# Optimization experiments

Hardware: AMD Instinct MI355X
Metric: run time of the kernel (lower is better)

Reference implementation:

```python
import jax, jax.numpy as jnp
import numpy as np
from jax import lax

SUB_NO = 20
T_NO = 401       # odd, so padding=T_NO//2 preserves length
N_E = 2000
N_I = 200
T_DATA = 50000
EXP_NO = 81
HID_NO = 6


def _conv1d(x, kern, pad, groups=1):
    # x: [N, C, L], kern: [O, I, K]; torch-style cross-correlation
    return lax.conv_general_dilated(
        x, kern, window_strides=(1,), padding=[(pad, pad)],
        dimension_numbers=('NCH', 'OIH', 'NCH'), feature_group_count=groups)


def setup_inputs() -> dict:
    key = jax.random.key(0)
    ks = jax.random.split(key, 8)
    rng = np.random.default_rng(0)

    # binary-tree dendrite: parent(j) = (j-1)//2; C_den[parent, child] = 1
    C_den = np.zeros((SUB_NO, SUB_NO), np.float32)
    for j in range(1, SUB_NO):
        C_den[(j - 1) // 2, j] = 1.0

    # one-hot synapse -> subunit assignment matrices
    C_syn_e = np.zeros((SUB_NO, N_E), np.float32)
    C_syn_e[rng.integers(0, SUB_NO, N_E), np.arange(N_E)] = 1.0
    C_syn_i = np.zeros((SUB_NO, N_I), np.float32)
    C_syn_i[rng.integers(0, SUB_NO, N_I), np.arange(N_I)] = 1.0

    # Gaussian-bump temporal basis (fixed buffer)
    raw = np.arange(T_NO, dtype=np.float32)
    points = np.arange(0, 5 * EXP_NO, 5, dtype=np.float32)
    exp_basis = np.exp(-(raw[None, :] - points[:, None]) ** 2 / 30.0).astype(np.float32)

    f32 = jnp.float32
    return {
        'S_e': jax.random.uniform(ks[0], (T_DATA, N_E), dtype=f32),
        'S_i': jax.random.uniform(ks[1], (T_DATA, N_I), dtype=f32),
        'Z': jax.random.bernoulli(ks[2], 0.02, (T_DATA,)).astype(f32),
        'W_syn': jax.random.normal(ks[3], (SUB_NO, 2), dtype=f32) * 0.01,
        'Tau_syn': jnp.ones((SUB_NO, 2), f32) * 3.0,
        'Delta_syn': jnp.ones((SUB_NO, 2), f32),
        'W_sub': jnp.ones((SUB_NO,), f32) * 0.1,
        'W_spk': jnp.ones((1,), f32),
        'Tau_spk': jnp.ones((1,), f32) * 3.0,
        'Theta': jnp.zeros((SUB_NO,), f32),
        'W_root_1': jax.random.normal(ks[4], (HID_NO, 1, EXP_NO), dtype=f32) * 0.01,
        'W_root_2': jax.random.normal(ks[5], (1, HID_NO, EXP_NO), dtype=f32) * 0.01,
        'C_den': jnp.asarray(C_den),
        'C_syn_e': jnp.asarray(C_syn_e),
        'C_syn_i': jnp.asarray(C_syn_i),
        'exp_basis': jnp.asarray(exp_basis),
    }


def reference(S_e, S_i, Z, W_syn, Tau_syn, Delta_syn, W_sub, W_spk, Tau_spk,
              Theta, W_root_1, W_root_2, C_den, C_syn_e, C_syn_i, exp_basis):
    T = S_e.shape[0]
    sub_no = C_den.shape[0]
    T_no = exp_basis.shape[1]

    # ---- spike_convolve ----
    syn_e = S_e @ C_syn_e.T          # [T, sub]
    syn_i = S_i @ C_syn_i.T          # [T, sub]

    t = jnp.arange(T_no, dtype=S_e.dtype)[None, :]            # [1, T_no]
    t_e = jnp.maximum(t - Delta_syn[:, 0:1], 0.0)
    t_i = jnp.maximum(t - Delta_syn[:, 1:2], 0.0)
    t_tau_e = t_e / Tau_syn[:, 0:1] ** 2
    t_tau_i = t_i / Tau_syn[:, 1:2] ** 2
    full_e_kern = t_tau_e * jnp.exp(-t_tau_e) * W_syn[:, 0:1] ** 2     # [sub, T_no]
    full_i_kern = -(t_tau_i * jnp.exp(-t_tau_i) * W_syn[:, 1:2] ** 2)  # [sub, T_no]

    ke = jnp.flip(full_e_kern, 1)[:, None, :]   # [sub, 1, T_no]
    ki = jnp.flip(full_i_kern, 1)[:, None, :]

    pad_e = jnp.pad(syn_e, ((T_no - 1, 0), (0, 0))).T[None]  # [1, sub, T+T_no-1]
    pad_i = jnp.pad(syn_i, ((T_no - 1, 0), (0, 0))).T[None]
    filt_e = _conv1d(pad_e, ke, 0, groups=sub_no)[0].T        # [T, sub]
    filt_i = _conv1d(pad_i, ki, 0, groups=sub_no)[0].T
    syn = filt_e + filt_i
    out_filters = jnp.concatenate([full_e_kern, full_i_kern], axis=0)  # [2*sub, T_no]

    # ---- subunit tree recursion (children have larger indices than parents) ----
    root_kern_1 = jnp.flip(jnp.matmul(W_root_1, exp_basis), 2)  # [hid, 1, T_no]
    root_kern_2 = jnp.flip(jnp.matmul(W_root_2, exp_basis), 2)  # [1, hid, T_no]
    w2 = W_sub ** 2

    ns_out = jnp.zeros((T, sub_no), S_e.dtype)
    for i in range(sub_no - 1, 0, -1):
        child = ns_out @ (C_den[i] * w2)                 # [T]
        ns_out = ns_out.at[:, i].set(jnp.tanh(syn[:, i] + Theta[i] + child))

    # root subunit with 2-layer temporal conv head
    child = ns_out @ (C_den[0] * w2)
    ns_in = syn[:, 0] + Theta[0] + child
    h = jnp.tanh(ns_in)[None, None, :]                   # [1, 1, T]
    h = jnp.tanh(_conv1d(h, root_kern_1, T_no // 2))     # [1, hid, T]
    final_Z = jax.nn.sigmoid(_conv1d(h, root_kern_2, T_no // 2).reshape(-1))  # [T]

    # ---- spike-history filter on Z ----
    t1 = jnp.arange(T_no, dtype=S_e.dtype)
    t_tau = t1 / Tau_spk ** 2
    spk_kern = jnp.flip(t_tau * jnp.exp(-t_tau) * W_spk ** 2, 0)[None, None, :]
    pad_Z = jnp.pad(Z, (T_no, 0))[None, None, :]         # [1, 1, T+T_no]
    final_V = _conv1d(pad_Z, spk_kern, 0).reshape(-1)[:-1]   # [T]

    return (final_V, final_Z, out_filters)
```

## Files before the change

### kernel.cpp

```cpp
#include <hip/hip_runtime.h>
#include <math.h>

#define T_DATA 50000
#define N_E 2000
#define N_I 200
#define SUB_NO 20
#define T_NO 401
#define KP 404
#define EXP_NO 81
#define HID_NO 6
#define ROWS 16

#define WS_SYN_ET   0
#define WS_SYN_IT   1000000
#define WS_SYNT     2000000
#define WS_H0       3000000
#define WS_H        3050000
#define WS_PART     3350000
#define WS_KE       3650000
#define WS_KI       3658080
#define WS_K1       3666160
#define WS_K2       3668584
#define WS_SPK      3671008
#define WS_ASGE     3671412
#define WS_ASGI     3671924

__global__ __launch_bounds__(256) void k_prep(
    const float* __restrict__ W_syn, const float* __restrict__ Tau_syn,
    const float* __restrict__ Delta_syn, const float* __restrict__ W_spk,
    const float* __restrict__ Tau_spk, const float* __restrict__ W_root_1,
    const float* __restrict__ W_root_2, const float* __restrict__ C_syn_e,
    const float* __restrict__ C_syn_i, const float* __restrict__ exp_basis,
    float* __restrict__ ws, unsigned int* __restrict__ asg_e,
    unsigned int* __restrict__ asg_i, float* __restrict__ out_filters) {
  const int bid = blockIdx.x, tid = threadIdx.x;
  if (bid == 0) {
    for (int u = tid; u < 512; u += 256) {
      unsigned int p = 0;
      for (int jj = 0; jj < 4; ++jj) {
        const int e = u * 4 + jj;
        int a = 20;
        if (e < N_E) {
          a = 0;
          for (int s = 0; s < SUB_NO; ++s) if (C_syn_e[s * N_E + e] > 0.5f) a = s;
        }
        p |= (unsigned int)a << (8 * jj);
      }
      asg_e[u] = p;
    }
  } else if (bid == 1) {
    for (int u = tid; u < 64; u += 256) {
      unsigned int p = 0;
      for (int jj = 0; jj < 4; ++jj) {
        const int e = u * 4 + jj;
        int a = 20;
        if (e < N_I) {
          a = 0;
          for (int s = 0; s < SUB_NO; ++s) if (C_syn_i[s * N_I + e] > 0.5f) a = s;
        }
        p |= (unsigned int)a << (8 * jj);
      }
      asg_i[u] = p;
    }
  } else if (bid == 2) {
    const float tau = Tau_spk[0], w = W_spk[0];
    const float it2 = 1.f / (tau * tau);
    for (int t = tid; t < KP; t += 256) {
      float v = 0.f;
      if (t < T_NO) { float tt = (float)t * it2; v = tt * __expf(-tt) * w * w; }
      ws[WS_SPK + t] = v;
    }
  } else if (bid < 3 + SUB_NO) {
    const int s = bid - 3;
    const float we = W_syn[s * 2], wi = W_syn[s * 2 + 1];
    const float te = Tau_syn[s * 2], ti = Tau_syn[s * 2 + 1];
    const float de = Delta_syn[s * 2], di = Delta_syn[s * 2 + 1];
    const float ie2 = 1.f / (te * te), ii2 = 1.f / (ti * ti);
    for (int t = tid; t < KP; t += 256) {
      float ve = 0.f, vi = 0.f;
      if (t < T_NO) {
        float xe = fmaxf((float)t - de, 0.f) * ie2;
        float xi = fmaxf((float)t - di, 0.f) * ii2;
        ve = xe * __expf(-xe) * we * we;
        vi = -(xi * __expf(-xi) * wi * wi);
        out_filters[s * T_NO + t] = ve;
        out_filters[(SUB_NO + s) * T_NO + t] = vi;
      }
      ws[WS_KE + s * KP + t] = ve;
      ws[WS_KI + s * KP + t] = vi;
    }
  } else {
    const int h = bid - (3 + SUB_NO);
    for (int t = tid; t < KP; t += 256) {
      float v1 = 0.f, v2 = 0.f;
      if (t < T_NO) {
        for (int b = 0; b < EXP_NO; ++b) {
          float bb = exp_basis[b * T_NO + t];
          v1 = fmaf(W_root_1[h * EXP_NO + b], bb, v1);
          v2 = fmaf(W_root_2[h * EXP_NO + b], bb, v2);
        }
      }
      ws[WS_K1 + h * KP + t] = v1;
      ws[WS_K2 + h * KP + t] = v2;
    }
  }
}

#define TSTR 260
__global__ __launch_bounds__(256) void k_seg(
    const float* __restrict__ S_e, const float* __restrict__ S_i,
    const unsigned int* __restrict__ asg_e, const unsigned int* __restrict__ asg_i,
    float* __restrict__ syn_eT, float* __restrict__ syn_iT) {
  __shared__ __align__(16) float tile[ROWS * TSTR];
  __shared__ float acc[256 * 21];
  __shared__ unsigned int asgl[512 + 64];
  const int tid = threadIdx.x;
  const int t0 = blockIdx.x * ROWS;
  const int r = tid & 15;
  const int sub = tid >> 4;
  float* __restrict__ myacc = acc + tid * 21;

  for (int i = tid; i < 512; i += 256) asgl[i] = asg_e[i];
  if (tid < 64) asgl[512 + tid] = asg_i[tid];
  #pragma unroll
  for (int i = 0; i < 21; ++i) myacc[i] = 0.f;
  __syncthreads();

  for (int ch = 0; ch < 8; ++ch) {
    #pragma unroll
    for (int i = 0; i < 4; ++i) {
      const int g = tid + i * 256;
      const int row = g >> 6, c4 = g & 63;
      const int col = ch * 256 + c4 * 4;
      float4 v = make_float4(0.f, 0.f, 0.f, 0.f);
      if (col < N_E) v = *(const float4*)(S_e + (size_t)(t0 + row) * N_E + col);
      *(float4*)(tile + row * TSTR + c4 * 4) = v;
    }
    __syncthreads();
    #pragma unroll
    for (int j = 0; j < 4; ++j) {
      const float4 v = *(const float4*)(tile + r * TSTR + sub * 16 + j * 4);
      const unsigned int a = asgl[ch * 64 + sub * 4 + j];
      myacc[a & 255] += v.x;
      myacc[(a >> 8) & 255] += v.y;
      myacc[(a >> 16) & 255] += v.z;
      myacc[a >> 24] += v.w;
    }
    __syncthreads();
  }
  for (int o = tid; o < ROWS * SUB_NO; o += 256) {
    const int row = o & 15, s = o >> 4;
    float sum = 0.f;
    #pragma unroll
    for (int c = 0; c < 16; ++c) sum += acc[(c * 16 + row) * 21 + s];
    syn_eT[s * T_DATA + t0 + row] = sum;
  }
  __syncthreads();
  #pragma unroll
  for (int i = 0; i < 21; ++i) myacc[i] = 0.f;

  #pragma unroll
  for (int i = 0; i < 4; ++i) {
    const int g = tid + i * 256;
    const int row = g >> 6, c4 = g & 63;
    const int col = c4 * 4;
    float4 v = make_float4(0.f, 0.f, 0.f, 0.f);
    if (col < N_I) v = *(const float4*)(S_i + (size_t)(t0 + row) * N_I + col);
    *(float4*)(tile + row * TSTR + c4 * 4) = v;
  }
  __syncthreads();
  #pragma unroll
  for (int j = 0; j < 4; ++j) {
    const float4 v = *(const float4*)(tile + r * TSTR + sub * 16 + j * 4);
    const unsigned int a = asgl[512 + sub * 4 + j];
    myacc[a & 255] += v.x;
    myacc[(a >> 8) & 255] += v.y;
    myacc[(a >> 16) & 255] += v.z;
    myacc[a >> 24] += v.w;
  }
  __syncthreads();
  for (int o = tid; o < ROWS * SUB_NO; o += 256) {
    const int row = o & 15, s = o >> 4;
    float sum = 0.f;
    #pragma unroll
    for (int c = 0; c < 16; ++c) sum += acc[(c * 16 + row) * 21 + s];
    syn_iT[s * T_DATA + t0 + row] = sum;
  }
}

template <int NOUT>
__device__ __forceinline__ void conv_acc(const float* __restrict__ xl,
                                         const float* __restrict__ kg,
                                         int lt, float* __restrict__ acc) {
  constexpr int NW = NOUT + 4;
  float xw[NW];
  #pragma unroll
  for (int r = 0; r < NW / 4; ++r) {
    float4 v = *(const float4*)(xl + lt + 400 + 4 * r);
    xw[4 * r + 0] = v.x; xw[4 * r + 1] = v.y;
    xw[4 * r + 2] = v.z; xw[4 * r + 3] = v.w;
  }
  const float* kp = kg;
  for (int g = 0; g < 100; ++g) {
    float4 kv = *(const float4*)kp; kp += 4;
    float kw[4] = {kv.x, kv.y, kv.z, kv.w};
    #pragma unroll
    for (int m = 0; m < 4; ++m)
      #pragma unroll
      for (int j = 0; j < NOUT; ++j)
        acc[j] = fmaf(kw[m], xw[4 + j - m], acc[j]);
    #pragma unroll
    for (int i = NW - 1; i >= 4; --i) xw[i] = xw[i - 4];
    float4 nv = *(const float4*)(xl + lt + 396 - 4 * g);
    xw[0] = nv.x; xw[1] = nv.y; xw[2] = nv.z; xw[3] = nv.w;
  }
  {
    float4 kv = *(const float4*)kp;
    float kw[4] = {kv.x, kv.y, kv.z, kv.w};
    #pragma unroll
    for (int m = 0; m < 4; ++m)
      #pragma unroll
      for (int j = 0; j < NOUT; ++j)
        acc[j] = fmaf(kw[m], xw[4 + j - m], acc[j]);
  }
}

__device__ __forceinline__ void fill_tile(float* __restrict__ xl,
                                          const float* __restrict__ X,
                                          int o, int n) {
  for (int i = threadIdx.x; i < n; i += blockDim.x) {
    int g = o + i;
    xl[i] = (g >= 0 && g < T_DATA) ? X[g] : 0.f;
  }
}

__global__ __launch_bounds__(256) void k_syn_conv(
    const float* __restrict__ syn_eT, const float* __restrict__ syn_iT,
    const float* __restrict__ ws, float* __restrict__ synT) {
  const int s = blockIdx.y;
  const int t0 = blockIdx.x * 2048;
  __shared__ __align__(16) float xe[2456];
  __shared__ __align__(16) float xi[2456];
  fill_tile(xe, syn_eT + s * T_DATA, t0 - 404, 2452);
  fill_tile(xi, syn_iT + s * T_DATA, t0 - 404, 2452);
  __syncthreads();
  const int lt = threadIdx.x * 8;
  float acc[8] = {0, 0, 0, 0, 0, 0, 0, 0};
  conv_acc<8>(xe, ws + WS_KE + s * KP, lt, acc);
  conv_acc<8>(xi, ws + WS_KI + s * KP, lt, acc);
  const int t = t0 + lt;
  #pragma unroll
  for (int j = 0; j < 8; ++j)
    if (t + j < T_DATA) synT[s * T_DATA + t + j] = acc[j];
}

__global__ __launch_bounds__(256) void k_tree(
    const float* __restrict__ synT, const float* __restrict__ Theta,
    const float* __restrict__ W_sub, float* __restrict__ h0) {
  const int t = blockIdx.x * 256 + threadIdx.x;
  if (t >= T_DATA) return;
  float ns[SUB_NO];
  #pragma unroll
  for (int i = SUB_NO - 1; i >= 1; --i) {
    float x = synT[i * T_DATA + t] + Theta[i];
    const int c1 = 2 * i + 1, c2 = 2 * i + 2;
    if (c1 < SUB_NO) { float w = W_sub[c1]; x = fmaf(w * w, ns[c1], x); }
    if (c2 < SUB_NO) { float w = W_sub[c2]; x = fmaf(w * w, ns[c2], x); }
    ns[i] = tanhf(x);
  }
  const float w1 = W_sub[1], w2 = W_sub[2];
  const float x0 = synT[t] + Theta[0] + w1 * w1 * ns[1] + w2 * w2 * ns[2];
  h0[t] = tanhf(x0);
}

__global__ __launch_bounds__(256) void k_root1(
    const float* __restrict__ h0, const float* __restrict__ ws,
    float* __restrict__ h_ws) {
  const int c = blockIdx.y;
  const int t0 = blockIdx.x * 1024;
  __shared__ __align__(16) float xt[1432];
  fill_tile(xt, h0, t0 + 200 - 404, 1428);
  __syncthreads();
  const int lt = threadIdx.x * 4;
  float acc[4] = {0, 0, 0, 0};
  conv_acc<4>(xt, ws + WS_K1 + c * KP, lt, acc);
  const int t = t0 + lt;
  #pragma unroll
  for (int j = 0; j < 4; ++j)
    if (t + j < T_DATA) h_ws[c * T_DATA + t + j] = tanhf(acc[j]);
}

__global__ __launch_bounds__(256) void k_root2(
    const float* __restrict__ h_ws, const float* __restrict__ ws,
    float* __restrict__ part) {
  const int c = blockIdx.y;
  const int t0 = blockIdx.x * 1024;
  __shared__ __align__(16) float xt[1432];
  fill_tile(xt, h_ws + c * T_DATA, t0 + 200 - 404, 1428);
  __syncthreads();
  const int lt = threadIdx.x * 4;
  float acc[4] = {0, 0, 0, 0};
  conv_acc<4>(xt, ws + WS_K2 + c * KP, lt, acc);
  const int t = t0 + lt;
  #pragma unroll
  for (int j = 0; j < 4; ++j)
    if (t + j < T_DATA) part[c * T_DATA + t + j] = acc[j];
}

__global__ __launch_bounds__(256) void k_comb(
    const float* __restrict__ part, float* __restrict__ outZ) {
  const int t = blockIdx.x * 256 + threadIdx.x;
  if (t >= T_DATA) return;
  float v = 0.f;
  #pragma unroll
  for (int c = 0; c < HID_NO; ++c) v += part[c * T_DATA + t];
  outZ[t] = 1.f / (1.f + __expf(-v));
}

__global__ __launch_bounds__(256) void k_spk(
    const float* __restrict__ Z, const float* __restrict__ ws,
    float* __restrict__ outV) {
  const int t0 = blockIdx.x * 1024;
  __shared__ __align__(16) float xt[1432];
  fill_tile(xt, Z, t0 - 1 - 404, 1428);
  __syncthreads();
  const int lt = threadIdx.x * 4;
  float acc[4] = {0, 0, 0, 0};
  conv_acc<4>(xt, ws + WS_SPK, lt, acc);
  const int t = t0 + lt;
  #pragma unroll
  for (int j = 0; j < 4; ++j)
    if (t + j < T_DATA) outV[t + j] = acc[j];
}

extern "C" void kernel_launch(void* const* d_in, const int* in_sizes, int n_in,
                              void* d_out, int out_size, void* d_ws, size_t ws_size,
                              hipStream_t stream) {
  const float* S_e      = (const float*)d_in[0];
  const float* S_i      = (const float*)d_in[1];
  const float* Z        = (const float*)d_in[2];
  const float* W_syn    = (const float*)d_in[3];
  const float* Tau_syn  = (const float*)d_in[4];
  const float* Delta_syn= (const float*)d_in[5];
  const float* W_sub    = (const float*)d_in[6];
  const float* W_spk    = (const float*)d_in[7];
  const float* Tau_spk  = (const float*)d_in[8];
  const float* Theta    = (const float*)d_in[9];
  const float* W_root_1 = (const float*)d_in[10];
  const float* W_root_2 = (const float*)d_in[11];
  const float* C_syn_e  = (const float*)d_in[13];
  const float* C_syn_i  = (const float*)d_in[14];
  const float* exp_basis= (const float*)d_in[15];

  float* ws = (float*)d_ws;
  unsigned int* asg_e = (unsigned int*)(ws + WS_ASGE);
  unsigned int* asg_i = (unsigned int*)(ws + WS_ASGI);
  float* out = (float*)d_out;

  k_prep<<<3 + SUB_NO + HID_NO, 256, 0, stream>>>(
      W_syn, Tau_syn, Delta_syn, W_spk, Tau_spk, W_root_1, W_root_2,
      C_syn_e, C_syn_i, exp_basis, ws, asg_e, asg_i, out + 2 * T_DATA);

  k_seg<<<T_DATA / ROWS, 256, 0, stream>>>(
      S_e, S_i, asg_e, asg_i, ws + WS_SYN_ET, ws + WS_SYN_IT);

  k_syn_conv<<<dim3(25, SUB_NO), 256, 0, stream>>>(
      ws + WS_SYN_ET, ws + WS_SYN_IT, ws, ws + WS_SYNT);

  k_tree<<<(T_DATA + 255) / 256, 256, 0, stream>>>(
      ws + WS_SYNT, Theta, W_sub, ws + WS_H0);

  k_root1<<<dim3(49, HID_NO), 256, 0, stream>>>(ws + WS_H0, ws, ws + WS_H);

  k_root2<<<dim3(49, HID_NO), 256, 0, stream>>>(ws + WS_H, ws, ws + WS_PART);

  k_comb<<<(T_DATA + 255) / 256, 256, 0, stream>>>(ws + WS_PART, out + T_DATA);

  k_spk<<<49, 256, 0, stream>>>(Z, ws, out);
}
```

Baseline: 191.5 us.

## Load S_e directly to registers, split syn conv by e/i, merge spike conv, fast tanh

The segment-sum kernel now reads S_e/S_i rows straight from global memory into registers instead of staging through a shared tile, which removes two barriers per chunk. The synaptic conv is split into separate excitatory and inhibitory blocks to double parallelism, and the tree kernel sums the two results. The spike-history conv is folded into the root2 launch as an extra grid row, and tanh and sigmoid use fast exp/rcp intrinsics. Trade-offs: the direct global loads are less coalesced across threads, the split conv needs an extra intermediate buffer, and the fast math lowers accuracy.

```diff
diff --git a/kernel.cpp b/kernel.cpp
--- a/kernel.cpp
+++ b/kernel.cpp
@@ -13,17 +13,23 @@
 
 #define WS_SYN_ET   0
 #define WS_SYN_IT   1000000
-#define WS_SYNT     2000000
-#define WS_H0       3000000
-#define WS_H        3050000
-#define WS_PART     3350000
-#define WS_KE       3650000
-#define WS_KI       3658080
-#define WS_K1       3666160
-#define WS_K2       3668584
-#define WS_SPK      3671008
-#define WS_ASGE     3671412
-#define WS_ASGI     3671924
+#define WS_SYNTE    2000000
+#define WS_SYNTI    3000000
+#define WS_H0       4000000
+#define WS_H        4050000
+#define WS_PART     4350000
+#define WS_KE       4650000
+#define WS_KI       4658080
+#define WS_K1       4666160
+#define WS_K2       4668584
+#define WS_SPK      4671008
+#define WS_ASGE     4671412
+#define WS_ASGI     4671924
+
+__device__ __forceinline__ float ftanh(float x) {
+  float e = __expf(2.f * x);
+  return 1.f - 2.f * __builtin_amdgcn_rcpf(e + 1.f);
+}
 
 __global__ __launch_bounds__(256) void k_prep(
     const float* __restrict__ W_syn, const float* __restrict__ Tau_syn,
@@ -106,18 +112,16 @@
   }
 }
 
-#define TSTR 260
 __global__ __launch_bounds__(256) void k_seg(
     const float* __restrict__ S_e, const float* __restrict__ S_i,
     const unsigned int* __restrict__ asg_e, const unsigned int* __restrict__ asg_i,
     float* __restrict__ syn_eT, float* __restrict__ syn_iT) {
-  __shared__ __align__(16) float tile[ROWS * TSTR];
   __shared__ float acc[256 * 21];
   __shared__ unsigned int asgl[512 + 64];
   const int tid = threadIdx.x;
   const int t0 = blockIdx.x * ROWS;
-  const int r = tid & 15;
-  const int sub = tid >> 4;
+  const int r = tid >> 4;
+  const int sub = tid & 15;
   float* __restrict__ myacc = acc + tid * 21;
 
   for (int i = tid; i < 512; i += 256) asgl[i] = asg_e[i];
@@ -126,64 +130,63 @@
   for (int i = 0; i < 21; ++i) myacc[i] = 0.f;
   __syncthreads();
 
+  const float* rowp = S_e + (size_t)(t0 + r) * N_E;
+  #pragma unroll
   for (int ch = 0; ch < 8; ++ch) {
-    #pragma unroll
-    for (int i = 0; i < 4; ++i) {
-      const int g = tid + i * 256;
-      const int row = g >> 6, c4 = g & 63;
-      const int col = ch * 256 + c4 * 4;
-      float4 v = make_float4(0.f, 0.f, 0.f, 0.f);
-      if (col < N_E) v = *(const float4*)(S_e + (size_t)(t0 + row) * N_E + col);
-      *(float4*)(tile + row * TSTR + c4 * 4) = v;
-    }
-    __syncthreads();
+    const int col0 = ch * 256 + sub * 16;
+    float4 v[4];
     #pragma unroll
     for (int j = 0; j < 4; ++j) {
-      const float4 v = *(const float4*)(tile + r * TSTR + sub * 16 + j * 4);
+      const int col = col0 + j * 4;
+      v[j] = (col + 4 <= N_E) ? *(const float4*)(rowp + col)
+                              : make_float4(0.f, 0.f, 0.f, 0.f);
+    }
+    #pragma unroll
+    for (int j = 0; j < 4; ++j) {
       const unsigned int a = asgl[ch * 64 + sub * 4 + j];
-      myacc[a & 255] += v.x;
-      myacc[(a >> 8) & 255] += v.y;
-      myacc[(a >> 16) & 255] += v.z;
-      myacc[a >> 24] += v.w;
-    }
-    __syncthreads();
-  }
+      myacc[a & 255]         += v[j].x;
+      myacc[(a >> 8) & 255]  += v[j].y;
+      myacc[(a >> 16) & 255] += v[j].z;
+      myacc[a >> 24]         += v[j].w;
+    }
+  }
+  __syncthreads();
   for (int o = tid; o < ROWS * SUB_NO; o += 256) {
     const int row = o & 15, s = o >> 4;
     float sum = 0.f;
     #pragma unroll
-    for (int c = 0; c < 16; ++c) sum += acc[(c * 16 + row) * 21 + s];
+    for (int c = 0; c < 16; ++c) sum += acc[(row * 16 + c) * 21 + s];
     syn_eT[s * T_DATA + t0 + row] = sum;
   }
   __syncthreads();
   #pragma unroll
   for (int i = 0; i < 21; ++i) myacc[i] = 0.f;
 
-  #pragma unroll
-  for (int i = 0; i < 4; ++i) {
-    const int g = tid + i * 256;
-    const int row = g >> 6, c4 = g & 63;
-    const int col = c4 * 4;
-    float4 v = make_float4(0.f, 0.f, 0.f, 0.f);
-    if (col < N_I) v = *(const float4*)(S_i + (size_t)(t0 + row) * N_I + col);
-    *(float4*)(tile + row * TSTR + c4 * 4) = v;
-  }
-  __syncthreads();
-  #pragma unroll
-  for (int j = 0; j < 4; ++j) {
-    const float4 v = *(const float4*)(tile + r * TSTR + sub * 16 + j * 4);
-    const unsigned int a = asgl[512 + sub * 4 + j];
-    myacc[a & 255] += v.x;
-    myacc[(a >> 8) & 255] += v.y;
-    myacc[(a >> 16) & 255] += v.z;
-    myacc[a >> 24] += v.w;
+  {
+    const float* rowpI = S_i + (size_t)(t0 + r) * N_I;
+    const int col0 = sub * 16;
+    float4 v[4];
+    #pragma unroll
+    for (int j = 0; j < 4; ++j) {
+      const int col = col0 + j * 4;
+      v[j] = (col + 4 <= N_I) ? *(const float4*)(rowpI + col)
+                              : make_float4(0.f, 0.f, 0.f, 0.f);
+    }
+    #pragma unroll
+    for (int j = 0; j < 4; ++j) {
+      const unsigned int a = asgl[512 + sub * 4 + j];
+      myacc[a & 255]         += v[j].x;
+      myacc[(a >> 8) & 255]  += v[j].y;
+      myacc[(a >> 16) & 255] += v[j].z;
+      myacc[a >> 24]         += v[j].w;
+    }
   }
   __syncthreads();
   for (int o = tid; o < ROWS * SUB_NO; o += 256) {
     const int row = o & 15, s = o >> 4;
     float sum = 0.f;
     #pragma unroll
-    for (int c = 0; c < 16; ++c) sum += acc[(c * 16 + row) * 21 + s];
+    for (int c = 0; c < 16; ++c) sum += acc[(row * 16 + c) * 21 + s];
     syn_iT[s * T_DATA + t0 + row] = sum;
   }
 }
@@ -236,41 +239,44 @@
 
 __global__ __launch_bounds__(256) void k_syn_conv(
     const float* __restrict__ syn_eT, const float* __restrict__ syn_iT,
-    const float* __restrict__ ws, float* __restrict__ synT) {
+    const float* __restrict__ ws, float* __restrict__ synTe,
+    float* __restrict__ synTi) {
   const int s = blockIdx.y;
+  const int ei = blockIdx.z;
   const int t0 = blockIdx.x * 2048;
-  __shared__ __align__(16) float xe[2456];
-  __shared__ __align__(16) float xi[2456];
-  fill_tile(xe, syn_eT + s * T_DATA, t0 - 404, 2452);
-  fill_tile(xi, syn_iT + s * T_DATA, t0 - 404, 2452);
+  const float* src = ei ? (syn_iT + s * T_DATA) : (syn_eT + s * T_DATA);
+  const float* kern = ws + (ei ? WS_KI : WS_KE) + s * KP;
+  float* dst = (ei ? synTi : synTe) + s * T_DATA;
+  __shared__ __align__(16) float xt[2456];
+  fill_tile(xt, src, t0 - 404, 2452);
   __syncthreads();
   const int lt = threadIdx.x * 8;
   float acc[8] = {0, 0, 0, 0, 0, 0, 0, 0};
-  conv_acc<8>(xe, ws + WS_KE + s * KP, lt, acc);
-  conv_acc<8>(xi, ws + WS_KI + s * KP, lt, acc);
+  conv_acc<8>(xt, kern, lt, acc);
   const int t = t0 + lt;
   #pragma unroll
   for (int j = 0; j < 8; ++j)
-    if (t + j < T_DATA) synT[s * T_DATA + t + j] = acc[j];
+    if (t + j < T_DATA) dst[t + j] = acc[j];
 }
 
 __global__ __launch_bounds__(256) void k_tree(
-    const float* __restrict__ synT, const float* __restrict__ Theta,
-    const float* __restrict__ W_sub, float* __restrict__ h0) {
+    const float* __restrict__ synTe, const float* __restrict__ synTi,
+    const float* __restrict__ Theta, const float* __restrict__ W_sub,
+    float* __restrict__ h0) {
   const int t = blockIdx.x * 256 + threadIdx.x;
   if (t >= T_DATA) return;
   float ns[SUB_NO];
   #pragma unroll
   for (int i = SUB_NO - 1; i >= 1; --i) {
-    float x = synT[i * T_DATA + t] + Theta[i];
+    float x = synTe[i * T_DATA + t] + synTi[i * T_DATA + t] + Theta[i];
     const int c1 = 2 * i + 1, c2 = 2 * i + 2;
     if (c1 < SUB_NO) { float w = W_sub[c1]; x = fmaf(w * w, ns[c1], x); }
     if (c2 < SUB_NO) { float w = W_sub[c2]; x = fmaf(w * w, ns[c2], x); }
-    ns[i] = tanhf(x);
+    ns[i] = ftanh(x);
   }
   const float w1 = W_sub[1], w2 = W_sub[2];
-  const float x0 = synT[t] + Theta[0] + w1 * w1 * ns[1] + w2 * w2 * ns[2];
-  h0[t] = tanhf(x0);
+  const float x0 = synTe[t] + synTi[t] + Theta[0] + w1 * w1 * ns[1] + w2 * w2 * ns[2];
+  h0[t] = ftanh(x0);
 }
 
 __global__ __launch_bounds__(256) void k_root1(
@@ -287,24 +293,35 @@
   const int t = t0 + lt;
   #pragma unroll
   for (int j = 0; j < 4; ++j)
-    if (t + j < T_DATA) h_ws[c * T_DATA + t + j] = tanhf(acc[j]);
-}
-
-__global__ __launch_bounds__(256) void k_root2(
-    const float* __restrict__ h_ws, const float* __restrict__ ws,
-    float* __restrict__ part) {
+    if (t + j < T_DATA) h_ws[c * T_DATA + t + j] = ftanh(acc[j]);
+}
+
+__global__ __launch_bounds__(256) void k_root2spk(
+    const float* __restrict__ h_ws, const float* __restrict__ Z,
+    const float* __restrict__ ws, float* __restrict__ part,
+    float* __restrict__ outV) {
   const int c = blockIdx.y;
   const int t0 = blockIdx.x * 1024;
   __shared__ __align__(16) float xt[1432];
-  fill_tile(xt, h_ws + c * T_DATA, t0 + 200 - 404, 1428);
-  __syncthreads();
   const int lt = threadIdx.x * 4;
   float acc[4] = {0, 0, 0, 0};
-  conv_acc<4>(xt, ws + WS_K2 + c * KP, lt, acc);
-  const int t = t0 + lt;
-  #pragma unroll
-  for (int j = 0; j < 4; ++j)
-    if (t + j < T_DATA) part[c * T_DATA + t + j] = acc[j];
+  if (c < HID_NO) {
+    fill_tile(xt, h_ws + c * T_DATA, t0 + 200 - 404, 1428);
+    __syncthreads();
+    conv_acc<4>(xt, ws + WS_K2 + c * KP, lt, acc);
+    const int t = t0 + lt;
+    #pragma unroll
+    for (int j = 0; j < 4; ++j)
+      if (t + j < T_DATA) part[c * T_DATA + t + j] = acc[j];
+  } else {
+    fill_tile(xt, Z, t0 - 1 - 404, 1428);
+    __syncthreads();
+    conv_acc<4>(xt, ws + WS_SPK, lt, acc);
+    const int t = t0 + lt;
+    #pragma unroll
+    for (int j = 0; j < 4; ++j)
+      if (t + j < T_DATA) outV[t + j] = acc[j];
+  }
 }
 
 __global__ __launch_bounds__(256) void k_comb(
@@ -314,23 +331,7 @@
   float v = 0.f;
   #pragma unroll
   for (int c = 0; c < HID_NO; ++c) v += part[c * T_DATA + t];
-  outZ[t] = 1.f / (1.f + __expf(-v));
-}
-
-__global__ __launch_bounds__(256) void k_spk(
-    const float* __restrict__ Z, const float* __restrict__ ws,
-    float* __restrict__ outV) {
-  const int t0 = blockIdx.x * 1024;
-  __shared__ __align__(16) float xt[1432];
-  fill_tile(xt, Z, t0 - 1 - 404, 1428);
-  __syncthreads();
-  const int lt = threadIdx.x * 4;
-  float acc[4] = {0, 0, 0, 0};
-  conv_acc<4>(xt, ws + WS_SPK, lt, acc);
-  const int t = t0 + lt;
-  #pragma unroll
-  for (int j = 0; j < 4; ++j)
-    if (t + j < T_DATA) outV[t + j] = acc[j];
+  outZ[t] = __builtin_amdgcn_rcpf(1.f + __expf(-v));
 }
 
 extern "C" void kernel_launch(void* const* d_in, const int* in_sizes, int n_in,
@@ -364,17 +365,16 @@
   k_seg<<<T_DATA / ROWS, 256, 0, stream>>>(
       S_e, S_i, asg_e, asg_i, ws + WS_SYN_ET, ws + WS_SYN_IT);
 
-  k_syn_conv<<<dim3(25, SUB_NO), 256, 0, stream>>>(
-      ws + WS_SYN_ET, ws + WS_SYN_IT, ws, ws + WS_SYNT);
+  k_syn_conv<<<dim3(25, SUB_NO, 2), 256, 0, stream>>>(
+      ws + WS_SYN_ET, ws + WS_SYN_IT, ws, ws + WS_SYNTE, ws + WS_SYNTI);
 
   k_tree<<<(T_DATA + 255) / 256, 256, 0, stream>>>(
-      ws + WS_SYNT, Theta, W_sub, ws + WS_H0);
+      ws + WS_SYNTE, ws + WS_SYNTI, Theta, W_sub, ws + WS_H0);
 
   k_root1<<<dim3(49, HID_NO), 256, 0, stream>>>(ws + WS_H0, ws, ws + WS_H);
 
-  k_root2<<<dim3(49, HID_NO), 256, 0, stream>>>(ws + WS_H, ws, ws + WS_PART);
+  k_root2spk<<<dim3(49, HID_NO + 1), 256, 0, stream>>>(
+      ws + WS_H, Z, ws, ws + WS_PART, out);
 
   k_comb<<<(T_DATA + 255) / 256, 256, 0, stream>>>(ws + WS_PART, out + T_DATA);
-
-  k_spk<<<49, 256, 0, stream>>>(Z, ws, out);
-}
+}
```

New measurement: 193.6 us (median of 2 runs). No clear change (+1.1%).
